# Optimization experiments

Hardware: AMD Instinct MI355X
Metric: run time of the kernel (lower is better)

Reference implementation:

```python
import jax, jax.numpy as jnp
import numpy as np

DIM = 64        # feature channels of x
HEADS = 4
POS_DIM = 3
NUM_IDS = 8
STR_IN = 512    # strength_linear input size
B, S, W = 4, 1024, 8   # batch, sequence (S1), source-views (S2)


def setup_inputs() -> dict:
    key = jax.random.key(0)
    ks = jax.random.split(key, 18)
    stdv = 1.0 / np.sqrt(DIM * DIM)  # embedding init per module
    d8 = DIM // 8
    u = lambda k, shp, s: jax.random.uniform(k, shp, jnp.float32, -s, s)
    return {
        "x": jax.random.normal(ks[0], (B, DIM, S, W), jnp.float32),
        "pos": jax.random.normal(ks[1], (B, S, POS_DIM), jnp.float32),
        "strength": jax.random.normal(ks[2], (STR_IN,), jnp.float32),
        "embed_id1": 3,
        "q_emb_w": u(ks[3], (NUM_IDS, DIM * DIM), stdv),
        "k_emb_w": u(ks[4], (NUM_IDS, DIM * DIM), stdv),
        "v_emb_w": u(ks[5], (NUM_IDS, DIM * DIM), stdv),
        "pos_w1": u(ks[6], (POS_DIM, POS_DIM), 1.0 / np.sqrt(POS_DIM)),
        "pos_b1": u(ks[7], (POS_DIM,), 1.0 / np.sqrt(POS_DIM)),
        "pos_w2": u(ks[8], (d8, POS_DIM), 1.0 / np.sqrt(POS_DIM)),
        "pos_b2": u(ks[9], (d8,), 1.0 / np.sqrt(POS_DIM)),
        "head_w": u(ks[10], (HEADS, d8), 1.0 / np.sqrt(d8)),
        "head_b": u(ks[11], (HEADS,), 1.0 / np.sqrt(d8)),
        "gate": jnp.ones((HEADS,), jnp.float32),
        "out_w": u(ks[12], (DIM, DIM), 1.0 / np.sqrt(DIM)),
        "out_b": u(ks[13], (DIM,), 1.0 / np.sqrt(DIM)),
        "str_w": u(ks[14], (DIM, STR_IN), 1.0 / np.sqrt(STR_IN)),
        "str_b": u(ks[15], (DIM,), 1.0 / np.sqrt(STR_IN)),
    }


def reference(x, pos, strength, embed_id1, q_emb_w, k_emb_w, v_emb_w,
              pos_w1, pos_b1, pos_w2, pos_b2, head_w, head_b, gate,
              out_w, out_b, str_w, str_b):
    # strength projection: Linear(512, dim)
    s = strength @ str_w.T + str_b                    # [dim]
    xt = jnp.transpose(x, (0, 2, 3, 1))               # [B, S, W, dim]
    qe = q_emb_w[embed_id1].reshape(DIM, DIM)
    ke = k_emb_w[embed_id1].reshape(DIM, DIM)
    ve = v_emb_w[embed_id1].reshape(DIM, DIM)

    def proj(emb):
        y = xt @ emb.T + s                            # [B, S, W, dim]
        # collapse (W, dim) -> (heads, head_dim), heads to axis 1
        y = y.reshape(B, S, HEADS, -1)
        return jnp.transpose(y, (0, 2, 1, 3))         # [B, H, S, hd]

    q, k, v = proj(qe), proj(ke), proj(ve)
    hd = q.shape[-1]
    attn = jax.nn.softmax(jnp.einsum("bhsd,bhtd->bhst", q, k) / np.sqrt(hd), axis=-1)

    # relative-position attention branch
    ph = jax.nn.relu(pos @ pos_w1.T + pos_b1) @ pos_w2.T + pos_b2   # [B, S, dim//8]
    diff = ph[:, :, None, :] - ph[:, None, :, :]                    # [B, S, S, dim//8]
    pos_attn = jnp.transpose(diff @ head_w.T + head_b, (0, 3, 1, 2))
    pos_attn = jax.nn.softmax(pos_attn, axis=-1)                    # [B, H, S, S]

    g = jax.nn.sigmoid(gate).reshape(1, -1, 1, 1)
    attn = (1.0 - g) * attn + g * pos_attn
    attn = attn / jnp.sum(attn, axis=-1, keepdims=True)

    out = jnp.einsum("bhst,bhtd->bhsd", attn, v)      # [B, H, S, hd]
    out = jnp.transpose(out, (0, 2, 1, 3)).reshape(B, S, W, DIM)
    return out @ out_w.T + out_b                      # [B, S, W, dim]
```

## Files before the change

### kernel.cpp

```cpp
#include <hip/hip_runtime.h>
#include <math.h>
#include <stdint.h>

#define B_ 4
#define S_ 1024
#define F_ 512
#define HD 128
#define SOFT_C 4.0f

typedef __attribute__((ext_vector_type(8))) short short8;
typedef __attribute__((ext_vector_type(4))) float f32x4;
typedef __attribute__((ext_vector_type(4))) unsigned int u32x4;
typedef __attribute__((ext_vector_type(2))) unsigned int u32x2;

__device__ __forceinline__ unsigned short f2bf(float f) {
    unsigned int u = __float_as_uint(f);
    u = (u + 0x7FFFu + ((u >> 16) & 1u)) >> 16;
    return (unsigned short)u;
}
__device__ __forceinline__ float bf2f(unsigned int s) {
    return __uint_as_float(s << 16);
}
__device__ __forceinline__ void pack_hilo(const float* v, u32x4& hi, u32x4& lo) {
    #pragma unroll
    for (int p = 0; p < 4; ++p) {
        unsigned int h0 = f2bf(v[2 * p]), h1 = f2bf(v[2 * p + 1]);
        float l0 = v[2 * p] - bf2f(h0), l1 = v[2 * p + 1] - bf2f(h1);
        hi[p] = h0 | (h1 << 16);
        lo[p] = (unsigned int)f2bf(l0) | ((unsigned int)f2bf(l1) << 16);
    }
}

__global__ __launch_bounds__(256) void k_qkv(
    const float* __restrict__ x, const int* __restrict__ embed_id,
    const float* __restrict__ qw, const float* __restrict__ kw,
    const float* __restrict__ vw,
    const float* __restrict__ strength, const float* __restrict__ str_w,
    const float* __restrict__ str_b,
    const float* __restrict__ pos, const float* __restrict__ pw1,
    const float* __restrict__ pb1, const float* __restrict__ pw2,
    const float* __restrict__ pb2, const float* __restrict__ head_w,
    unsigned short* __restrict__ yqh, unsigned short* __restrict__ ykh,
    unsigned short* __restrict__ yvt2,
    float* __restrict__ sv_g, float* __restrict__ xbar)
{
    __shared__ unsigned short whi[3][4096];
    __shared__ unsigned short wlo[3][4096];
    __shared__ float part_s[4][64];
    __shared__ float sv_s[64], svq_s[64];
    __shared__ float xr_s[4][8];
    __shared__ float red_s[4][4];
    __shared__ float inv_s[4];

    const int tid  = threadIdx.x;
    const int wv   = tid >> 6;
    const int lane = tid & 63;
    const int quad = lane >> 4;
    const int l15  = lane & 15;
    const float SCALE = 0.08838834764831845f;

    if (blockIdx.x >= 256) {
        const int bi = blockIdx.x - 256;
        const int b = bi >> 6, c = bi & 63;
        float w1_[9], b1_[3], w2_[24], b2_[8], hw_[32];
        #pragma unroll
        for (int i = 0; i < 9; ++i)  w1_[i] = pw1[i];
        #pragma unroll
        for (int i = 0; i < 3; ++i)  b1_[i] = pb1[i];
        #pragma unroll
        for (int i = 0; i < 24; ++i) w2_[i] = pw2[i];
        #pragma unroll
        for (int i = 0; i < 8; ++i)  b2_[i] = pb2[i];
        #pragma unroll
        for (int i = 0; i < 32; ++i) hw_[i] = head_w[i];

        float pv_[4][4];
        float ps[4] = {0.f, 0.f, 0.f, 0.f};
        #pragma unroll
        for (int rr = 0; rr < 4; ++rr) {
            const int s = tid * 4 + rr;
            float p0 = pos[(b * S_ + s) * 3 + 0];
            float p1 = pos[(b * S_ + s) * 3 + 1];
            float p2 = pos[(b * S_ + s) * 3 + 2];
            float h0 = fmaxf(0.f, p0 * w1_[0] + p1 * w1_[1] + p2 * w1_[2] + b1_[0]);
            float h1 = fmaxf(0.f, p0 * w1_[3] + p1 * w1_[4] + p2 * w1_[5] + b1_[1]);
            float h2 = fmaxf(0.f, p0 * w1_[6] + p1 * w1_[7] + p2 * w1_[8] + b1_[2]);
            float ph[8];
            #pragma unroll
            for (int o8 = 0; o8 < 8; ++o8)
                ph[o8] = h0 * w2_[o8 * 3] + h1 * w2_[o8 * 3 + 1]
                       + h2 * w2_[o8 * 3 + 2] + b2_[o8];
            #pragma unroll
            for (int h = 0; h < 4; ++h) {
                float A = 0.f;
                #pragma unroll
                for (int o8 = 0; o8 < 8; ++o8) A += ph[o8] * hw_[h * 8 + o8];
                pv_[rr][h] = __expf(-A - 1.0f);
                ps[h] += pv_[rr][h];
            }
        }
        #pragma unroll
        for (int h = 0; h < 4; ++h)
            #pragma unroll
            for (int off = 1; off < 64; off <<= 1)
                ps[h] += __shfl_xor(ps[h], off);
        if (lane == 0)
            #pragma unroll
            for (int h = 0; h < 4; ++h) red_s[wv][h] = ps[h];
        __syncthreads();
        if (tid < 4)
            inv_s[tid] = 1.f / (red_s[0][tid] + red_s[1][tid]
                              + red_s[2][tid] + red_s[3][tid]);
        __syncthreads();

        const float* xc = x + (size_t)b * 524288 + c * 8192;
        float acc[8] = {};
        #pragma unroll
        for (int rr = 0; rr < 4; ++rr) {
            const int s = tid * 4 + rr;
            f32x4 x0 = *(const f32x4*)(xc + s * 8);
            f32x4 x1 = *(const f32x4*)(xc + s * 8 + 4);
            float q0 = pv_[rr][0] * inv_s[0];
            float q1 = pv_[rr][1] * inv_s[1];
            float q2 = pv_[rr][2] * inv_s[2];
            float q3 = pv_[rr][3] * inv_s[3];
            acc[0] += q0 * x0[0]; acc[1] += q0 * x0[1];
            acc[2] += q1 * x0[2]; acc[3] += q1 * x0[3];
            acc[4] += q2 * x1[0]; acc[5] += q2 * x1[1];
            acc[6] += q3 * x1[2]; acc[7] += q3 * x1[3];
        }
        #pragma unroll
        for (int j = 0; j < 8; ++j)
            #pragma unroll
            for (int off = 1; off < 64; off <<= 1)
                acc[j] += __shfl_xor(acc[j], off);
        if (lane == 0)
            #pragma unroll
            for (int j = 0; j < 8; ++j) xr_s[wv][j] = acc[j];
        __syncthreads();
        if (tid < 8)
            xbar[(b * 8 + tid) * 64 + c] = xr_s[0][tid] + xr_s[1][tid]
                                         + xr_s[2][tid] + xr_s[3][tid];
        return;
    }

    const int id = embed_id[0];

    for (int cc = tid; cc < 1536; cc += 256) {
        const int m  = cc >> 9;
        const int e0 = (cc & 511) << 3;
        const float* src = (m == 0 ? qw : m == 1 ? kw : vw) + id * 4096 + e0;
        const float sc = (m == 0) ? SCALE : 1.0f;
        f32x4 a0 = *(const f32x4*)src;
        f32x4 a1 = *(const f32x4*)(src + 4);
        float v8[8] = {a0[0] * sc, a0[1] * sc, a0[2] * sc, a0[3] * sc,
                       a1[0] * sc, a1[1] * sc, a1[2] * sc, a1[3] * sc};
        u32x4 hi, lo;
        pack_hilo(v8, hi, lo);
        const int r = e0 >> 6, c = e0 & 63;
        const int off = ((r >> 4) * 2 + (c >> 5)) * 512
                      + ((c >> 3) & 3) * 128 + (r & 15) * 8;
        *(u32x4*)(&whi[m][off]) = hi;
        *(u32x4*)(&wlo[m][off]) = lo;
    }

    {
        const float* wrow = str_w + lane * 512 + wv * 128;
        const float* st   = strength + wv * 128;
        float a = 0.f;
        #pragma unroll
        for (int j4 = 0; j4 < 32; ++j4) {
            f32x4 wv4 = *(const f32x4*)(wrow + j4 * 4);
            f32x4 s4  = *(const f32x4*)(st + j4 * 4);
            a += wv4[0] * s4[0] + wv4[1] * s4[1] + wv4[2] * s4[2] + wv4[3] * s4[3];
        }
        part_s[wv][lane] = a;
    }
    __syncthreads();
    if (tid < 64) {
        float v = part_s[0][tid] + part_s[1][tid] + part_s[2][tid]
                + part_s[3][tid] + str_b[tid];
        sv_s[tid]  = v;
        svq_s[tid] = v * SCALE;
        if (blockIdx.x == 0) sv_g[tid] = v;
    }
    __syncthreads();

    float svq_l[4], sv_l[4];
    #pragma unroll
    for (int nt = 0; nt < 4; ++nt) {
        svq_l[nt] = svq_s[nt * 16 + l15];
        sv_l[nt]  = sv_s[nt * 16 + l15];
    }
    f32x4 svA[4];
    #pragma unroll
    for (int mt = 0; mt < 4; ++mt)
        svA[mt] = *(const f32x4*)&sv_s[mt * 16 + quad * 4];

    #pragma unroll
    for (int u = 0; u < 2; ++u) {
        const int r0   = (blockIdx.x * 2 + u) * 64 + wv * 16;
        const int b    = r0 >> 13;
        const int rloc = (r0 & 8191) + l15;
        const float* xb = x + (size_t)b * 524288;

        u32x4 xhi[2], xlo[2];
        #pragma unroll
        for (int kc = 0; kc < 2; ++kc) {
            float xv[8];
            #pragma unroll
            for (int j = 0; j < 8; ++j)
                xv[j] = xb[(kc * 32 + quad * 8 + j) * 8192 + rloc];
            pack_hilo(xv, xhi[kc], xlo[kc]);
        }

        int idxq[4];
        #pragma unroll
        for (int rr = 0; rr < 4; ++rr) {
            const int rl = quad * 4 + rr;
            const int w_ = rl & 7;
            const int s_loc = ((r0 & 8191) >> 3) + (rl >> 3);
            idxq[rr] = (b * 4 + (w_ >> 1)) * 131072 + s_loc * 128 + (w_ & 1) * 64 + l15;
        }

        const int row_g = r0 + l15;
        const int s_idx = (row_g >> 3) & 1023;
        const int w_idx = row_g & 7;
        const int bh    = b * 4 + (w_idx >> 1);
        const int dbase = (w_idx & 1) * 64;
        unsigned short* vtb = yvt2 + (size_t)bh * 131072 + (s_idx >> 6) * 8192
                            + (size_t)dbase * 64 + (s_idx & 63);

        #pragma unroll
        for (int mat = 0; mat < 2; ++mat) {
            const unsigned short* mh = whi[mat];
            const unsigned short* ml = wlo[mat];
            f32x4 acc[4] = {};
            #pragma unroll
            for (int kc = 0; kc < 2; ++kc)
                #pragma unroll
                for (int nt = 0; nt < 4; ++nt) {
                    const int off = (nt * 2 + kc) * 512 + quad * 128 + l15 * 8;
                    u32x4 ehi = *(const u32x4*)(mh + off);
                    u32x4 elo = *(const u32x4*)(ml + off);
                    acc[nt] = __builtin_amdgcn_mfma_f32_16x16x32_bf16(
                        __builtin_bit_cast(short8, xhi[kc]),
                        __builtin_bit_cast(short8, ehi), acc[nt], 0, 0, 0);
                    acc[nt] = __builtin_amdgcn_mfma_f32_16x16x32_bf16(
                        __builtin_bit_cast(short8, xlo[kc]),
                        __builtin_bit_cast(short8, ehi), acc[nt], 0, 0, 0);
                    acc[nt] = __builtin_amdgcn_mfma_f32_16x16x32_bf16(
                        __builtin_bit_cast(short8, xhi[kc]),
                        __builtin_bit_cast(short8, elo), acc[nt], 0, 0, 0);
                }
            unsigned short* y = (mat == 0 ? yqh : ykh);
            const float* svp = (mat == 0 ? svq_l : sv_l);
            #pragma unroll
            for (int nt = 0; nt < 4; ++nt)
                #pragma unroll
                for (int rr = 0; rr < 4; ++rr)
                    y[(size_t)idxq[rr] + nt * 16] = f2bf(acc[nt][rr] + svp[nt]);
        }

        {
            const unsigned short* mh = whi[2];
            const unsigned short* ml = wlo[2];
            f32x4 acc[4] = {};
            #pragma unroll
            for (int kc = 0; kc < 2; ++kc)
                #pragma unroll
                for (int mt = 0; mt < 4; ++mt) {
                    const int off = (mt * 2 + kc) * 512 + quad * 128 + l15 * 8;
                    u32x4 ehi = *(const u32x4*)(mh + off);
                    u32x4 elo = *(const u32x4*)(ml + off);
                    acc[mt] = __builtin_amdgcn_mfma_f32_16x16x32_bf16(
                        __builtin_bit_cast(short8, ehi),
                        __builtin_bit_cast(short8, xhi[kc]), acc[mt], 0, 0, 0);
                    acc[mt] = __builtin_amdgcn_mfma_f32_16x16x32_bf16(
                        __builtin_bit_cast(short8, ehi),
                        __builtin_bit_cast(short8, xlo[kc]), acc[mt], 0, 0, 0);
                    acc[mt] = __builtin_amdgcn_mfma_f32_16x16x32_bf16(
                        __builtin_bit_cast(short8, elo),
                        __builtin_bit_cast(short8, xhi[kc]), acc[mt], 0, 0, 0);
                }
            #pragma unroll
            for (int mt = 0; mt < 4; ++mt)
                #pragma unroll
                for (int rr = 0; rr < 4; ++rr) {
                    const int c = mt * 16 + quad * 4 + rr;
                    vtb[(size_t)c * 64] = f2bf(acc[mt][rr] + svA[mt][rr]);
                }
        }
    }
}

__global__ __launch_bounds__(256, 4) void k_attn(
    const unsigned short* __restrict__ yqh, const unsigned short* __restrict__ ykh,
    const unsigned short* __restrict__ yvt2,
    const float* __restrict__ xbar, const float* __restrict__ vw,
    const int* __restrict__ embed_id, const float* __restrict__ sv,
    const float* __restrict__ gate,
    const float* __restrict__ out_w, const float* __restrict__ out_b,
    float* __restrict__ out)
{
    __shared__ __align__(16) unsigned char smem_kv[35840];
    __shared__ float vbar_s[128];
    __shared__ float vbarP_s[128];
    __shared__ float lsq_s[2][2][16];

    unsigned short* kx = (unsigned short*)smem_kv;
    unsigned short* vx = (unsigned short*)(smem_kv + 17408);

    const int tid  = threadIdx.x;
    const int w    = tid >> 6;
    const int lane = tid & 63;
    const int quad = lane >> 4;
    const int l15  = lane & 15;
    const int bh = blockIdx.x & 15, qt = blockIdx.x >> 4;
    const int b = bh >> 2, h = bh & 3;
    const int s0 = qt * 32;
    const int qh = w >> 1;
    const int ts = w & 1;

    const unsigned short* ykb = ykh + (size_t)bh * 131072;
    const unsigned short* yvb = yvt2 + (size_t)bh * 131072;

    if (tid < 128) {
        const int c = tid & 63, wloc = tid >> 6;
        const float* ver = vw + embed_id[0] * 4096 + c * 64;
        const float* xbr = xbar + (b * 8 + h * 2 + wloc) * 64;
        float a = sv[c];
        #pragma unroll
        for (int j4 = 0; j4 < 16; ++j4) {
            f32x4 e4 = *(const f32x4*)(ver + j4 * 4);
            f32x4 x4 = *(const f32x4*)(xbr + j4 * 4);
            a += e4[0] * x4[0] + e4[1] * x4[1] + e4[2] * x4[2] + e4[3] * x4[3];
        }
        vbar_s[wloc * 64 + c] = a;
    }

    u32x4 qf[4];
    #pragma unroll
    for (int kc = 0; kc < 4; ++kc)
        qf[kc] = *(const u32x4*)(yqh + (size_t)bh * 131072
                 + (s0 + qh * 16 + l15) * 128 + kc * 32 + quad * 8);

    #pragma unroll
    for (int r = 0; r < 4; ++r) {
        const int off = r * 2048 + tid * 8;
        *(u32x4*)&kx[(off >> 7) * 136 + (off & 127)] =
            *(const u32x4*)(ykb + off);
        *(u32x4*)&vx[(off >> 6) * 72 + (off & 63)] =
            *(const u32x4*)(yvb + off);
    }
    __syncthreads();

    if (tid < 128) {
        const int seg = tid >> 6, dq = tid & 63;
        const float* wr = out_w + dq * 64;
        float a = 0.f;
        #pragma unroll
        for (int j4 = 0; j4 < 16; ++j4) {
            f32x4 w4 = *(const f32x4*)(wr + j4 * 4);
            f32x4 v4 = *(const f32x4*)&vbar_s[seg * 64 + j4 * 4];
            a += w4[0] * v4[0] + w4[1] * v4[1] + w4[2] * v4[2] + w4[3] * v4[3];
        }
        vbarP_s[seg * 64 + dq] = a;
    }

    f32x4 o[8] = {};
    float lsum = 0.f;
    const int srcA = ((quad & 1) << 5) + l15;

    for (int it = 0; it < 16; ++it) {
        u32x4 kst[4], vst[4];
        const bool pre = (it < 15);
        if (pre) {
            const unsigned short* ksrc = ykb + (it + 1) * 8192;
            const unsigned short* vsrc = yvb + (it + 1) * 8192;
            #pragma unroll
            for (int r = 0; r < 4; ++r)
                kst[r] = *(const u32x4*)(ksrc + r * 2048 + tid * 8);
            #pragma unroll
            for (int r = 0; r < 4; ++r)
                vst[r] = *(const u32x4*)(vsrc + r * 2048 + tid * 8);
        }

        f32x4 sa0 = {}, sa1 = {};
        #pragma unroll
        for (int kc = 0; kc < 4; ++kc) {
            u32x4 a0 = *(const u32x4*)&kx[(ts * 32 + l15) * 136 + kc * 32 + quad * 8];
            sa0 = __builtin_amdgcn_mfma_f32_16x16x32_bf16(
                __builtin_bit_cast(short8, a0),
                __builtin_bit_cast(short8, qf[kc]), sa0, 0, 0, 0);
        }
        #pragma unroll
        for (int kc = 0; kc < 4; ++kc) {
            u32x4 a1 = *(const u32x4*)&kx[(ts * 32 + 16 + l15) * 136 + kc * 32 + quad * 8];
            sa1 = __builtin_amdgcn_mfma_f32_16x16x32_bf16(
                __builtin_bit_cast(short8, a1),
                __builtin_bit_cast(short8, qf[kc]), sa1, 0, 0, 0);
        }

        float p0[4], p1[4];
        #pragma unroll
        for (int r = 0; r < 4; ++r) {
            p0[r] = __expf(sa0[r] - SOFT_C);
            p1[r] = __expf(sa1[r] - SOFT_C);
            lsum += p0[r] + p1[r];
        }

        unsigned int pk00 = (unsigned int)f2bf(p0[0]) | ((unsigned int)f2bf(p0[1]) << 16);
        unsigned int pk01 = (unsigned int)f2bf(p0[2]) | ((unsigned int)f2bf(p0[3]) << 16);
        unsigned int pk10 = (unsigned int)f2bf(p1[0]) | ((unsigned int)f2bf(p1[1]) << 16);
        unsigned int pk11 = (unsigned int)f2bf(p1[2]) | ((unsigned int)f2bf(p1[3]) << 16);
        unsigned int sel0 = (quad < 2) ? pk00 : pk10;
        unsigned int sel1 = (quad < 2) ? pk01 : pk11;
        u32x4 pf;
        pf[0] = (unsigned int)__shfl((int)sel0, srcA);
        pf[1] = (unsigned int)__shfl((int)sel1, srcA);
        pf[2] = (unsigned int)__shfl((int)sel0, srcA + 16);
        pf[3] = (unsigned int)__shfl((int)sel1, srcA + 16);

        #pragma unroll
        for (int dt = 0; dt < 8; ++dt) {
            u32x4 vf = *(const u32x4*)&vx[(dt * 16 + l15) * 72 + ts * 32 + quad * 8];
            o[dt] = __builtin_amdgcn_mfma_f32_16x16x32_bf16(
                __builtin_bit_cast(short8, vf),
                __builtin_bit_cast(short8, pf), o[dt], 0, 0, 0);
        }

        __syncthreads();
        if (pre) {
            #pragma unroll
            for (int r = 0; r < 4; ++r) {
                const int off = r * 2048 + tid * 8;
                *(u32x4*)&kx[(off >> 7) * 136 + (off & 127)] = kst[r];
            }
            #pragma unroll
            for (int r = 0; r < 4; ++r) {
                const int off = r * 2048 + tid * 8;
                *(u32x4*)&vx[(off >> 6) * 72 + (off & 63)] = vst[r];
            }
            __syncthreads();
        }
    }

    float* obuf = (float*)smem_kv;
    {
        float* ow_ = obuf + ((qh * 2 + ts) * 16 + l15) * 132;
        #pragma unroll
        for (int dt = 0; dt < 8; ++dt)
            *(f32x4*)(ow_ + dt * 16 + quad * 4) = o[dt];
    }
    lsum += __shfl_xor(lsum, 16);
    lsum += __shfl_xor(lsum, 32);
    if (quad == 0) lsq_s[qh][ts][l15] = lsum;
    __syncthreads();

    const float gf = 1.f / (1.f + __expf(-gate[h]));
    const float cf = (1.f - gf) / (lsq_s[qh][0][l15] + lsq_s[qh][1][l15]);
    const float* oa  = obuf + ((qh * 2 + 0) * 16 + l15) * 132;
    const float* obp = obuf + ((qh * 2 + 1) * 16 + l15) * 132;

    u32x4 bhi[2], blo[2];
    #pragma unroll
    for (int kc = 0; kc < 2; ++kc) {
        const int off = ts * 64 + kc * 32 + quad * 8;
        f32x4 a0 = *(const f32x4*)(oa + off);
        f32x4 a1 = *(const f32x4*)(oa + off + 4);
        f32x4 c0 = *(const f32x4*)(obp + off);
        f32x4 c1 = *(const f32x4*)(obp + off + 4);
        float yv[8] = {cf * (a0[0] + c0[0]), cf * (a0[1] + c0[1]),
                       cf * (a0[2] + c0[2]), cf * (a0[3] + c0[3]),
                       cf * (a1[0] + c1[0]), cf * (a1[1] + c1[1]),
                       cf * (a1[2] + c1[2]), cf * (a1[3] + c1[3])};
        pack_hilo(yv, bhi[kc], blo[kc]);
    }

    f32x4 acc[4] = {};
    #pragma unroll
    for (int kc = 0; kc < 2; ++kc)
        #pragma unroll
        for (int mt = 0; mt < 4; ++mt) {
            const float* wsrc2 = out_w + (mt * 16 + l15) * 64 + kc * 32 + quad * 8;
            f32x4 w0 = *(const f32x4*)wsrc2;
            f32x4 w1 = *(const f32x4*)(wsrc2 + 4);
            float wv8[8] = {w0[0], w0[1], w0[2], w0[3], w1[0], w1[1], w1[2], w1[3]};
            u32x4 ahi, alo;
            pack_hilo(wv8, ahi, alo);
            acc[mt] = __builtin_amdgcn_mfma_f32_16x16x32_bf16(
                __builtin_bit_cast(short8, ahi),
                __builtin_bit_cast(short8, bhi[kc]), acc[mt], 0, 0, 0);
            acc[mt] = __builtin_amdgcn_mfma_f32_16x16x32_bf16(
                __builtin_bit_cast(short8, ahi),
                __builtin_bit_cast(short8, blo[kc]), acc[mt], 0, 0, 0);
            acc[mt] = __builtin_amdgcn_mfma_f32_16x16x32_bf16(
                __builtin_bit_cast(short8, alo),
                __builtin_bit_cast(short8, bhi[kc]), acc[mt], 0, 0, 0);
        }

    const int w_seg = h * 2 + ts;
    const size_t rowb = ((size_t)(b * S_ + s0 + qh * 16 + l15) * 8 + w_seg) * 64;
    #pragma unroll
    for (int mt = 0; mt < 4; ++mt) {
        f32x4 vb   = *(const f32x4*)&vbarP_s[ts * 64 + mt * 16 + quad * 4];
        f32x4 bias = *(const f32x4*)(out_b + mt * 16 + quad * 4);
        f32x4 res;
        #pragma unroll
        for (int j = 0; j < 4; ++j) res[j] = acc[mt][j] + gf * vb[j] + bias[j];
        *(f32x4*)(out + rowb + mt * 16 + quad * 4) = res;
    }
}

extern "C" void kernel_launch(void* const* d_in, const int* in_sizes, int n_in,
                              void* d_out, int out_size, void* d_ws, size_t ws_size,
                              hipStream_t stream) {
    (void)in_sizes; (void)n_in; (void)out_size; (void)ws_size;
    const float* x        = (const float*)d_in[0];
    const float* pos      = (const float*)d_in[1];
    const float* strength = (const float*)d_in[2];
    const int*   embed_id = (const int*)d_in[3];
    const float* qw       = (const float*)d_in[4];
    const float* kw       = (const float*)d_in[5];
    const float* vw       = (const float*)d_in[6];
    const float* pw1      = (const float*)d_in[7];
    const float* pb1      = (const float*)d_in[8];
    const float* pw2      = (const float*)d_in[9];
    const float* pb2      = (const float*)d_in[10];
    const float* head_w   = (const float*)d_in[11];
    const float* gate     = (const float*)d_in[13];
    const float* out_w    = (const float*)d_in[14];
    const float* out_b    = (const float*)d_in[15];
    const float* str_w    = (const float*)d_in[16];
    const float* str_b    = (const float*)d_in[17];
    float* out = (float*)d_out;

    unsigned short* yqh   = (unsigned short*)d_ws;
    unsigned short* ykh   = yqh + 2097152;
    unsigned short* yvt2  = ykh + 2097152;
    float* sv   = (float*)(yvt2 + 2097152);
    float* xbar = sv + 64;

    k_qkv<<<512, 256, 0, stream>>>(x, embed_id, qw, kw, vw,
                                   strength, str_w, str_b,
                                   pos, pw1, pb1, pw2, pb2, head_w,
                                   yqh, ykh, yvt2, sv, xbar);
    k_attn<<<512, 256, 0, stream>>>(yqh, ykh, yvt2, xbar, vw, embed_id, sv,
                                    gate, out_w, out_b, out);
}
```

Before: 141.7 us.

## Split attention key tiles across eight waves per block

The attention kernel now launches 512 threads instead of 256, giving four waves per query half where there were two. Each wave handles a 16-key slice of every 64-key tile instead of 32 keys, and PV uses zero-padded P fragments for the unused half of the MFMA K dimension. Partial outputs from the extra waves are reduced through shared memory before the output projection, which only half the waves perform. The aim is more latency hiding and more parallel work per block, at the cost of wasted MFMA work in PV, an extra reduction pass with a barrier, and possibly fewer resident blocks per CU.

```diff
diff --git a/kernel.cpp b/kernel.cpp
--- a/kernel.cpp
+++ b/kernel.cpp
@@ -294,7 +294,7 @@
     }
 }
 
-__global__ __launch_bounds__(256, 4) void k_attn(
+__global__ __launch_bounds__(512, 4) void k_attn(
     const unsigned short* __restrict__ yqh, const unsigned short* __restrict__ ykh,
     const unsigned short* __restrict__ yvt2,
     const float* __restrict__ xbar, const float* __restrict__ vw,
@@ -303,10 +303,10 @@
     const float* __restrict__ out_w, const float* __restrict__ out_b,
     float* __restrict__ out)
 {
-    __shared__ __align__(16) unsigned char smem_kv[35840];
+    __shared__ __align__(16) unsigned char smem_kv[35856];
     __shared__ float vbar_s[128];
     __shared__ float vbarP_s[128];
-    __shared__ float lsq_s[2][2][16];
+    __shared__ float lsq_s[2][4][16];
 
     unsigned short* kx = (unsigned short*)smem_kv;
     unsigned short* vx = (unsigned short*)(smem_kv + 17408);
@@ -319,8 +319,8 @@
     const int bh = blockIdx.x & 15, qt = blockIdx.x >> 4;
     const int b = bh >> 2, h = bh & 3;
     const int s0 = qt * 32;
-    const int qh = w >> 1;
-    const int ts = w & 1;
+    const int qh = w >> 2;
+    const int ts = w & 3;
 
     const unsigned short* ykb = ykh + (size_t)bh * 131072;
     const unsigned short* yvb = yvt2 + (size_t)bh * 131072;
@@ -346,8 +346,8 @@
                  + (s0 + qh * 16 + l15) * 128 + kc * 32 + quad * 8);
 
     #pragma unroll
-    for (int r = 0; r < 4; ++r) {
-        const int off = r * 2048 + tid * 8;
+    for (int r = 0; r < 2; ++r) {
+        const int off = r * 4096 + tid * 8;
         *(u32x4*)&kx[(off >> 7) * 136 + (off & 127)] =
             *(const u32x4*)(ykb + off);
         *(u32x4*)&vx[(off >> 6) * 72 + (off & 63)] =
@@ -371,60 +371,50 @@
     f32x4 o[8] = {};
     float lsum = 0.f;
     const int srcA = ((quad & 1) << 5) + l15;
+    const int vcol = ts * 16 + (quad & 1) * 8;
 
     for (int it = 0; it < 16; ++it) {
-        u32x4 kst[4], vst[4];
+        u32x4 kst[2], vst[2];
         const bool pre = (it < 15);
         if (pre) {
             const unsigned short* ksrc = ykb + (it + 1) * 8192;
             const unsigned short* vsrc = yvb + (it + 1) * 8192;
             #pragma unroll
-            for (int r = 0; r < 4; ++r)
-                kst[r] = *(const u32x4*)(ksrc + r * 2048 + tid * 8);
-            #pragma unroll
-            for (int r = 0; r < 4; ++r)
-                vst[r] = *(const u32x4*)(vsrc + r * 2048 + tid * 8);
-        }
-
-        f32x4 sa0 = {}, sa1 = {};
+            for (int r = 0; r < 2; ++r)
+                kst[r] = *(const u32x4*)(ksrc + r * 4096 + tid * 8);
+            #pragma unroll
+            for (int r = 0; r < 2; ++r)
+                vst[r] = *(const u32x4*)(vsrc + r * 4096 + tid * 8);
+        }
+
+        f32x4 sa = {};
         #pragma unroll
         for (int kc = 0; kc < 4; ++kc) {
-            u32x4 a0 = *(const u32x4*)&kx[(ts * 32 + l15) * 136 + kc * 32 + quad * 8];
-            sa0 = __builtin_amdgcn_mfma_f32_16x16x32_bf16(
+            u32x4 a0 = *(const u32x4*)&kx[(ts * 16 + l15) * 136 + kc * 32 + quad * 8];
+            sa = __builtin_amdgcn_mfma_f32_16x16x32_bf16(
                 __builtin_bit_cast(short8, a0),
-                __builtin_bit_cast(short8, qf[kc]), sa0, 0, 0, 0);
-        }
-        #pragma unroll
-        for (int kc = 0; kc < 4; ++kc) {
-            u32x4 a1 = *(const u32x4*)&kx[(ts * 32 + 16 + l15) * 136 + kc * 32 + quad * 8];
-            sa1 = __builtin_amdgcn_mfma_f32_16x16x32_bf16(
-                __builtin_bit_cast(short8, a1),
-                __builtin_bit_cast(short8, qf[kc]), sa1, 0, 0, 0);
-        }
-
-        float p0[4], p1[4];
+                __builtin_bit_cast(short8, qf[kc]), sa, 0, 0, 0);
+        }
+
+        float p0[4];
         #pragma unroll
         for (int r = 0; r < 4; ++r) {
-            p0[r] = __expf(sa0[r] - SOFT_C);
-            p1[r] = __expf(sa1[r] - SOFT_C);
-            lsum += p0[r] + p1[r];
-        }
-
+            p0[r] = __expf(sa[r] - SOFT_C);
+            lsum += p0[r];
+        }
         unsigned int pk00 = (unsigned int)f2bf(p0[0]) | ((unsigned int)f2bf(p0[1]) << 16);
         unsigned int pk01 = (unsigned int)f2bf(p0[2]) | ((unsigned int)f2bf(p0[3]) << 16);
-        unsigned int pk10 = (unsigned int)f2bf(p1[0]) | ((unsigned int)f2bf(p1[1]) << 16);
-        unsigned int pk11 = (unsigned int)f2bf(p1[2]) | ((unsigned int)f2bf(p1[3]) << 16);
-        unsigned int sel0 = (quad < 2) ? pk00 : pk10;
-        unsigned int sel1 = (quad < 2) ? pk01 : pk11;
+
         u32x4 pf;
-        pf[0] = (unsigned int)__shfl((int)sel0, srcA);
-        pf[1] = (unsigned int)__shfl((int)sel1, srcA);
-        pf[2] = (unsigned int)__shfl((int)sel0, srcA + 16);
-        pf[3] = (unsigned int)__shfl((int)sel1, srcA + 16);
+        pf[0] = (unsigned int)__shfl((int)pk00, srcA);
+        pf[1] = (unsigned int)__shfl((int)pk01, srcA);
+        pf[2] = (unsigned int)__shfl((int)pk00, srcA + 16);
+        pf[3] = (unsigned int)__shfl((int)pk01, srcA + 16);
+        if (quad >= 2) { pf[0] = 0; pf[1] = 0; pf[2] = 0; pf[3] = 0; }
 
         #pragma unroll
         for (int dt = 0; dt < 8; ++dt) {
-            u32x4 vf = *(const u32x4*)&vx[(dt * 16 + l15) * 72 + ts * 32 + quad * 8];
+            u32x4 vf = *(const u32x4*)&vx[(dt * 16 + l15) * 72 + vcol];
             o[dt] = __builtin_amdgcn_mfma_f32_16x16x32_bf16(
                 __builtin_bit_cast(short8, vf),
                 __builtin_bit_cast(short8, pf), o[dt], 0, 0, 0);
@@ -433,13 +423,13 @@
         __syncthreads();
         if (pre) {
             #pragma unroll
-            for (int r = 0; r < 4; ++r) {
-                const int off = r * 2048 + tid * 8;
+            for (int r = 0; r < 2; ++r) {
+                const int off = r * 4096 + tid * 8;
                 *(u32x4*)&kx[(off >> 7) * 136 + (off & 127)] = kst[r];
             }
             #pragma unroll
-            for (int r = 0; r < 4; ++r) {
-                const int off = r * 2048 + tid * 8;
+            for (int r = 0; r < 2; ++r) {
+                const int off = r * 4096 + tid * 8;
                 *(u32x4*)&vx[(off >> 6) * 72 + (off & 63)] = vst[r];
             }
             __syncthreads();
@@ -447,8 +437,8 @@
     }
 
     float* obuf = (float*)smem_kv;
-    {
-        float* ow_ = obuf + ((qh * 2 + ts) * 16 + l15) * 132;
+    if (ts >= 2) {
+        float* ow_ = obuf + ((qh * 2 + (ts - 2)) * 16 + l15) * 132;
         #pragma unroll
         for (int dt = 0; dt < 8; ++dt)
             *(f32x4*)(ow_ + dt * 16 + quad * 4) = o[dt];
@@ -457,59 +447,72 @@
     lsum += __shfl_xor(lsum, 32);
     if (quad == 0) lsq_s[qh][ts][l15] = lsum;
     __syncthreads();
-
-    const float gf = 1.f / (1.f + __expf(-gate[h]));
-    const float cf = (1.f - gf) / (lsq_s[qh][0][l15] + lsq_s[qh][1][l15]);
-    const float* oa  = obuf + ((qh * 2 + 0) * 16 + l15) * 132;
-    const float* obp = obuf + ((qh * 2 + 1) * 16 + l15) * 132;
-
-    u32x4 bhi[2], blo[2];
-    #pragma unroll
-    for (int kc = 0; kc < 2; ++kc) {
-        const int off = ts * 64 + kc * 32 + quad * 8;
-        f32x4 a0 = *(const f32x4*)(oa + off);
-        f32x4 a1 = *(const f32x4*)(oa + off + 4);
-        f32x4 c0 = *(const f32x4*)(obp + off);
-        f32x4 c1 = *(const f32x4*)(obp + off + 4);
-        float yv[8] = {cf * (a0[0] + c0[0]), cf * (a0[1] + c0[1]),
-                       cf * (a0[2] + c0[2]), cf * (a0[3] + c0[3]),
-                       cf * (a1[0] + c1[0]), cf * (a1[1] + c1[1]),
-                       cf * (a1[2] + c1[2]), cf * (a1[3] + c1[3])};
-        pack_hilo(yv, bhi[kc], blo[kc]);
-    }
-
-    f32x4 acc[4] = {};
-    #pragma unroll
-    for (int kc = 0; kc < 2; ++kc)
+    if (ts < 2) {
+        float* ow_ = obuf + ((qh * 2 + ts) * 16 + l15) * 132;
+        #pragma unroll
+        for (int dt = 0; dt < 8; ++dt) {
+            f32x4 pr = *(const f32x4*)(ow_ + dt * 16 + quad * 4);
+            o[dt] += pr;
+            *(f32x4*)(ow_ + dt * 16 + quad * 4) = o[dt];
+        }
+    }
+    __syncthreads();
+
+    if (ts < 2) {
+        const float gf = 1.f / (1.f + __expf(-gate[h]));
+        const float cf = (1.f - gf) / (lsq_s[qh][0][l15] + lsq_s[qh][1][l15]
+                                     + lsq_s[qh][2][l15] + lsq_s[qh][3][l15]);
+        const float* oa  = obuf + ((qh * 2 + 0) * 16 + l15) * 132;
+        const float* obp = obuf + ((qh * 2 + 1) * 16 + l15) * 132;
+
+        u32x4 bhi[2], blo[2];
+        #pragma unroll
+        for (int kc = 0; kc < 2; ++kc) {
+            const int off = ts * 64 + kc * 32 + quad * 8;
+            f32x4 a0 = *(const f32x4*)(oa + off);
+            f32x4 a1 = *(const f32x4*)(oa + off + 4);
+            f32x4 c0 = *(const f32x4*)(obp + off);
+            f32x4 c1 = *(const f32x4*)(obp + off + 4);
+            float yv[8] = {cf * (a0[0] + c0[0]), cf * (a0[1] + c0[1]),
+                           cf * (a0[2] + c0[2]), cf * (a0[3] + c0[3]),
+                           cf * (a1[0] + c1[0]), cf * (a1[1] + c1[1]),
+                           cf * (a1[2] + c1[2]), cf * (a1[3] + c1[3])};
+            pack_hilo(yv, bhi[kc], blo[kc]);
+        }
+
+        f32x4 acc[4] = {};
+        #pragma unroll
+        for (int kc = 0; kc < 2; ++kc)
+            #pragma unroll
+            for (int mt = 0; mt < 4; ++mt) {
+                const float* wsrc2 = out_w + (mt * 16 + l15) * 64 + kc * 32 + quad * 8;
+                f32x4 w0 = *(const f32x4*)wsrc2;
+                f32x4 w1 = *(const f32x4*)(wsrc2 + 4);
+                float wv8[8] = {w0[0], w0[1], w0[2], w0[3], w1[0], w1[1], w1[2], w1[3]};
+                u32x4 ahi, alo;
+                pack_hilo(wv8, ahi, alo);
+                acc[mt] = __builtin_amdgcn_mfma_f32_16x16x32_bf16(
+                    __builtin_bit_cast(short8, ahi),
+                    __builtin_bit_cast(short8, bhi[kc]), acc[mt], 0, 0, 0);
+                acc[mt] = __builtin_amdgcn_mfma_f32_16x16x32_bf16(
+                    __builtin_bit_cast(short8, ahi),
+                    __builtin_bit_cast(short8, blo[kc]), acc[mt], 0, 0, 0);
+                acc[mt] = __builtin_amdgcn_mfma_f32_16x16x32_bf16(
+                    __builtin_bit_cast(short8, alo),
+                    __builtin_bit_cast(short8, bhi[kc]), acc[mt], 0, 0, 0);
+            }
+
+        const int w_seg = h * 2 + ts;
+        const size_t rowb = ((size_t)(b * S_ + s0 + qh * 16 + l15) * 8 + w_seg) * 64;
         #pragma unroll
         for (int mt = 0; mt < 4; ++mt) {
-            const float* wsrc2 = out_w + (mt * 16 + l15) * 64 + kc * 32 + quad * 8;
-            f32x4 w0 = *(const f32x4*)wsrc2;
-            f32x4 w1 = *(const f32x4*)(wsrc2 + 4);
-            float wv8[8] = {w0[0], w0[1], w0[2], w0[3], w1[0], w1[1], w1[2], w1[3]};
-            u32x4 ahi, alo;
-            pack_hilo(wv8, ahi, alo);
-            acc[mt] = __builtin_amdgcn_mfma_f32_16x16x32_bf16(
-                __builtin_bit_cast(short8, ahi),
-                __builtin_bit_cast(short8, bhi[kc]), acc[mt], 0, 0, 0);
-            acc[mt] = __builtin_amdgcn_mfma_f32_16x16x32_bf16(
-                __builtin_bit_cast(short8, ahi),
-                __builtin_bit_cast(short8, blo[kc]), acc[mt], 0, 0, 0);
-            acc[mt] = __builtin_amdgcn_mfma_f32_16x16x32_bf16(
-                __builtin_bit_cast(short8, alo),
-                __builtin_bit_cast(short8, bhi[kc]), acc[mt], 0, 0, 0);
-        }
-
-    const int w_seg = h * 2 + ts;
-    const size_t rowb = ((size_t)(b * S_ + s0 + qh * 16 + l15) * 8 + w_seg) * 64;
-    #pragma unroll
-    for (int mt = 0; mt < 4; ++mt) {
-        f32x4 vb   = *(const f32x4*)&vbarP_s[ts * 64 + mt * 16 + quad * 4];
-        f32x4 bias = *(const f32x4*)(out_b + mt * 16 + quad * 4);
-        f32x4 res;
-        #pragma unroll
-        for (int j = 0; j < 4; ++j) res[j] = acc[mt][j] + gf * vb[j] + bias[j];
-        *(f32x4*)(out + rowb + mt * 16 + quad * 4) = res;
+            f32x4 vb   = *(const f32x4*)&vbarP_s[ts * 64 + mt * 16 + quad * 4];
+            f32x4 bias = *(const f32x4*)(out_b + mt * 16 + quad * 4);
+            f32x4 res;
+            #pragma unroll
+            for (int j = 0; j < 4; ++j) res[j] = acc[mt][j] + gf * vb[j] + bias[j];
+            *(f32x4*)(out + rowb + mt * 16 + quad * 4) = res;
+        }
     }
 }
 
@@ -546,6 +549,6 @@
                                    strength, str_w, str_b,
                                    pos, pw1, pb1, pw2, pb2, head_w,
                                    yqh, ykh, yvt2, sv, xbar);
-    k_attn<<<512, 256, 0, stream>>>(yqh, ykh, yvt2, xbar, vw, embed_id, sv,
+    k_attn<<<512, 512, 0, stream>>>(yqh, ykh, yvt2, xbar, vw, embed_id, sv,
                                     gate, out_w, out_b, out);
 }
```

Result: slower. 146.0 us (+3.0%).
